# Kernel tuning notes

Hardware: AMD Instinct MI355X
Metric: run time of the kernel (lower is better)

## Reference

```python
import jax, jax.numpy as jnp
import numpy as np


def _bilinear(img, gy, gx):
    # img: (H,W); gy,gx: normalized grid coords in [-1,1] (torch grid_sample,
    # bilinear, zeros padding, align_corners=False semantics)
    H, W = img.shape
    y = ((gy + 1.0) * H - 1.0) * 0.5
    x = ((gx + 1.0) * W - 1.0) * 0.5
    y0 = jnp.floor(y); x0 = jnp.floor(x)
    y1 = y0 + 1.0; x1 = x0 + 1.0
    wy1 = y - y0; wx1 = x - x0
    wy0 = 1.0 - wy1; wx0 = 1.0 - wx1

    def gather(yy, xx):
        valid = (yy >= 0) & (yy < H) & (xx >= 0) & (xx < W)
        yc = jnp.clip(yy, 0, H - 1).astype(jnp.int32)
        xc = jnp.clip(xx, 0, W - 1).astype(jnp.int32)
        return jnp.where(valid, img[yc, xc], 0.0)

    return (wy0 * wx0 * gather(y0, x0) + wy0 * wx1 * gather(y0, x1)
            + wy1 * wx0 * gather(y1, x0) + wy1 * wx1 * gather(y1, x1))


_sample = jax.vmap(_bilinear)  # over frames


def setup_inputs() -> dict:
    key = jax.random.key(0)
    ks = jax.random.split(key, 10)
    nframe, batchsize = 16, 1
    H, W = 512, 640
    hp, wp = H - 128, W - 128
    # C/C_back hold pixel coordinates: channel 2i -> y in [0,H], 2i+1 -> x in [0,W]
    scale = jnp.tile(jnp.array([H, W], jnp.float32), nframe)  # (2*nframe,)
    return {
        "y_pred": jax.random.normal(ks[0], (1, nframe - 1, hp, wp), jnp.float32),
        "inp1": jax.random.normal(ks[1], (1, 2, H, W), jnp.float32),
        "inp2": jax.random.normal(ks[2], (1, 2 * nframe, H, W), jnp.float32),
        "inp2_back": jax.random.normal(ks[3], (1, 2 * nframe, H, W), jnp.float32),
        "inp7": 0.1 * jax.random.normal(ks[4], (1, 9 * (nframe - 1)), jnp.float32),
        "inp6": jax.random.normal(ks[5], (1, hp, wp), jnp.float32),
        "inp77": 0.1 * jax.random.normal(ks[6], (1, 9), jnp.float32),
        "nframe": nframe,
        "batchsize": batchsize,
        "C": jax.random.uniform(ks[7], (1, H, W, 2 * nframe), jnp.float32) * scale,
        "C_back": jax.random.uniform(ks[8], (1, H, W, 2 * nframe), jnp.float32) * scale,
        "reg": 1,
        "P1": 1,
        "P2": 1,
    }


def reference(y_pred, inp1, inp2, inp2_back, inp7, inp6, inp77, nframe,
              batchsize, C, C_back, reg, P1, P2):
    # Original torch code is only well-defined for batchsize == 1.
    _, _, H, W = inp1.shape
    hp, wp = y_pred.shape[2], y_pred.shape[3]
    PAD = 64
    dt = y_pred.dtype

    # zero-padded warped-field stacks
    y_pred1 = jnp.zeros((nframe - 1, H, W), dt).at[:, PAD:PAD + hp, PAD:PAD + wp].set(y_pred[0])
    y_pred2 = jnp.zeros((H, W), dt).at[PAD:PAD + hp, PAD:PAD + wp].set(inp6[0])

    # per-frame homography params: inp5 (9, nframe+1), last column zeros
    inp5 = jnp.concatenate([inp77[0][:, None], inp7[0].reshape(9, nframe - 1),
                            jnp.zeros((9, 1), dt)], axis=1)
    a = inp5[0] + 1.0  # (nframe+1,)
    b = inp5[3]
    c = inp5[6]

    # grids: C[..., 2i] -> y, C[..., 2i+1] -> x, normalized to [-1,1]
    Cr = jnp.moveaxis(C[0].reshape(H, W, nframe, 2), 2, 0)       # (nframe,H,W,2)
    Cb = jnp.moveaxis(C_back[0].reshape(H, W, nframe, 2), 2, 0)
    gy = (Cr[..., 0] - H / 2) / (H / 2)
    gx = (Cr[..., 1] - W / 2) / (W / 2)
    gby = (Cb[..., 0] - H / 2) / (H / 2)
    gbx = (Cb[..., 1] - W / 2) / (W / 2)

    warp5 = _sample(y_pred1, gy[:nframe - 1], gx[:nframe - 1])   # (nframe-1,H,W)
    warp6 = _sample(y_pred1, gby[1:nframe], gbx[1:nframe])       # (nframe-1,H,W)

    zero = jnp.zeros((1, H, W), dt)
    warp5f = jnp.concatenate([warp5, zero])        # frame nframe-1 has no forward warp
    warp6f = jnp.concatenate([zero, warp6])        # frame 0 has no backward warp
    prev = jnp.concatenate([y_pred2[None], y_pred1])   # i==0 uses y_pred2, else y_pred1[i-1]
    nxt = jnp.concatenate([y_pred1, zero])             # last frame term is zero

    inp2_r = inp2[0].reshape(nframe, 2, H, W)
    back_r = inp2_back[0].reshape(nframe, 2, H, W)

    ai, bi, ci = a[:nframe, None, None], b[:nframe, None, None], c[:nframe, None, None]
    an, bn, cn = a[1:, None, None], b[1:, None, None], c[1:, None, None]

    diff0 = (ai * inp1[0, 1] + bi * inp1[0, 0] + ci + prev
             - (an * inp2_r[:, 1] + bn * inp2_r[:, 0] + cn + warp5f))
    diff1 = (ai * back_r[:, 1] + bi * back_r[:, 0] + ci + warp6f
             - (an * inp1[0, 1] + bn * inp1[0, 0] + cn + nxt))

    row0 = jnp.mean(diff0.reshape(nframe, -1) ** 2, axis=1)
    row1 = jnp.mean(diff1.reshape(nframe, -1) ** 2, axis=1)
    return jnp.mean(0.5 * (row0 + row1))
```

## Files before the change

kernel.cpp:

```cpp
#include <hip/hip_runtime.h>

#define HH 512
#define WW 640
#define HP 384
#define WP 512
#define PAD 64
#define NF 16
#define HW (HH*WW)
#define PXB 128
#define NPH 8
#define NBLK (HW/PXB)
#define CSTR 34

__device__ __forceinline__ float ntload(const float* p) {
    return __builtin_nontemporal_load(p);
}

__device__ __forceinline__ float row_pair(const float* __restrict__ yp, int fbase,
                                          int iy, int ix, float wx0, float wx1) {
    if ((unsigned)iy >= HP) return 0.f;
    const float* row = yp + (size_t)(fbase + iy) * WP;
    float v0 = ((unsigned)ix      < WP) ? row[ix]     : 0.f;
    float v1 = ((unsigned)(ix+1) < WP) ? row[ix + 1] : 0.f;
    return wx0 * v0 + wx1 * v1;
}

__device__ __forceinline__ float bsample(const float* __restrict__ yp, int f, float Cy, float Cx) {
    float gy = (Cy - 256.0f) / 256.0f;
    float gx = (Cx - 320.0f) / 320.0f;
    float y = ((gy + 1.0f) * 512.0f - 1.0f) * 0.5f;
    float x = ((gx + 1.0f) * 640.0f - 1.0f) * 0.5f;
    float y0f = floorf(y), x0f = floorf(x);
    float wy1 = y - y0f, wx1 = x - x0f;
    float wy0 = 1.0f - wy1, wx0 = 1.0f - wx1;
    int y0 = (int)y0f, x0 = (int)x0f;
    int fbase = f * HP;
    int iy0 = y0 - PAD, ix0 = x0 - PAD;
    float r0 = row_pair(yp, fbase, iy0,     ix0, wx0, wx1);
    float r1 = row_pair(yp, fbase, iy0 + 1, ix0, wx0, wx1);
    return wy0 * r0 + wy1 * r1;
}

__device__ __forceinline__ void coef(const float* __restrict__ inp7,
                                     const float* __restrict__ inp77,
                                     int k, float& a, float& b, float& c) {
    if (k == 0)      { a = inp77[0] + 1.0f;  b = inp77[3];     c = inp77[6];     }
    else if (k <= 15){ a = inp7[k-1] + 1.0f; b = inp7[45+k-1]; c = inp7[90+k-1]; }
    else             { a = 1.0f;             b = 0.0f;         c = 0.0f;         }
}

__global__ __launch_bounds__(256) void verloss_main(
    const float* __restrict__ y_pred,
    const float* __restrict__ inp1,
    const float* __restrict__ inp2,
    const float* __restrict__ inp2b,
    const float* __restrict__ inp7,
    const float* __restrict__ inp6,
    const float* __restrict__ inp77,
    const float* __restrict__ C,
    const float* __restrict__ Cb,
    double* __restrict__ partial)
{
    __shared__ float sC [PXB * CSTR];
    __shared__ float sCb[PXB * CSTR];
    __shared__ double sdata[4];

    const int tid  = threadIdx.x;
    const int pxl  = tid >> 1;
    const int kloc = tid & 1;
    const int p    = blockIdx.x * PXB + pxl;

    {
        const float2* gC  = reinterpret_cast<const float2*>(C  + (size_t)blockIdx.x * PXB * 32);
        const float2* gCb = reinterpret_cast<const float2*>(Cb + (size_t)blockIdx.x * PXB * 32);
        #pragma unroll
        for (int i = 0; i < 8; ++i) {
            int f2 = tid + i * 256;
            int spx = f2 >> 4, sj = f2 & 15;
            float2 v  = gC [f2];
            float2 vb = gCb[f2];
            *reinterpret_cast<float2*>(&sC [spx * CSTR + 2 * sj]) = v;
            *reinterpret_cast<float2*>(&sCb[spx * CSTR + 2 * sj]) = vb;
        }
    }

    int y = p / WW, x = p - y * WW;
    int iy = y - PAD, ix = x - PAD;
    bool inpad = ((unsigned)iy < HP) && ((unsigned)ix < WP);
    int padoff = iy * WP + ix;
    float A = inp1[HW + p];
    float B = inp1[p];

    float acc = 0.f;
    __syncthreads();

    for (int g = 0; g < NPH; ++g) {
        int k = 2 * g + kloc;

        float ak, bk, ck, an, bn, cn;
        coef(inp7, inp77, k,     ak, bk, ck);
        coef(inp7, inp77, k + 1, an, bn, cn);

        float prev;
        if (k == 0) prev = inpad ? inp6[padoff] : 0.f;
        else        prev = inpad ? y_pred[(size_t)((k-1)*HP)*WP + padoff] : 0.f;
        float nxt = (k < NF-1 && inpad) ? y_pred[(size_t)(k*HP)*WP + padoff] : 0.f;

        float w5 = 0.f, w6 = 0.f;
        if (k < NF-1) {
            float2 gg = *reinterpret_cast<const float2*>(&sC [pxl * CSTR + 2 * k]);
            w5 = bsample(y_pred, k, gg.x, gg.y);
        }
        if (k >= 1) {
            float2 gg = *reinterpret_cast<const float2*>(&sCb[pxl * CSTR + 2 * k]);
            w6 = bsample(y_pred, k - 1, gg.x, gg.y);
        }

        float i2hi = ntload(inp2  + (size_t)(2*k+1)*HW + p);
        float i2lo = ntload(inp2  + (size_t)(2*k  )*HW + p);
        float ibhi = ntload(inp2b + (size_t)(2*k+1)*HW + p);
        float iblo = ntload(inp2b + (size_t)(2*k  )*HW + p);

        float d0 = ak*A + bk*B + ck + prev - (an*i2hi + bn*i2lo + cn + w5);
        float d1 = ak*ibhi + bk*iblo + ck + w6 - (an*A + bn*B + cn + nxt);
        acc += d0*d0 + d1*d1;

        if (g < NPH - 1) __syncthreads();
    }

    double v = (double)acc;
    #pragma unroll
    for (int off = 32; off > 0; off >>= 1) v += __shfl_down(v, off, 64);
    int wid = tid >> 6, lane = tid & 63;
    if (lane == 0) sdata[wid] = v;
    __syncthreads();
    if (tid == 0)
        partial[blockIdx.x] = sdata[0] + sdata[1] + sdata[2] + sdata[3];
}

__global__ __launch_bounds__(1024) void verloss_finalize(
    const double* __restrict__ partial, int n, float* __restrict__ out)
{
    double v = 0.0;
    for (int i = threadIdx.x; i < n; i += 1024) v += partial[i];
    #pragma unroll
    for (int off = 32; off > 0; off >>= 1) v += __shfl_down(v, off, 64);
    __shared__ double sdata[16];
    int wid = threadIdx.x >> 6, lane = threadIdx.x & 63;
    if (lane == 0) sdata[wid] = v;
    __syncthreads();
    if (threadIdx.x == 0) {
        double s = 0.0;
        #pragma unroll
        for (int i = 0; i < 16; ++i) s += sdata[i];
        out[0] = (float)(s * (0.5 / ((double)NF * HW)));
    }
}

extern "C" void kernel_launch(void* const* d_in, const int* in_sizes, int n_in,
                              void* d_out, int out_size, void* d_ws, size_t ws_size,
                              hipStream_t stream) {
    const float* y_pred = (const float*)d_in[0];
    const float* inp1   = (const float*)d_in[1];
    const float* inp2   = (const float*)d_in[2];
    const float* inp2b  = (const float*)d_in[3];
    const float* inp7   = (const float*)d_in[4];
    const float* inp6   = (const float*)d_in[5];
    const float* inp77  = (const float*)d_in[6];
    const float* C      = (const float*)d_in[9];
    const float* Cb     = (const float*)d_in[10];
    float* out = (float*)d_out;
    double* partial = (double*)d_ws;

    verloss_main<<<NBLK, 256, 0, stream>>>(y_pred, inp1, inp2, inp2b, inp7,
                                           inp6, inp77, C, Cb, partial);
    verloss_finalize<<<1, 1024, 0, stream>>>(partial, NBLK, out);
}
```

Baseline: 136.4 us.

## Vectorize bilinear row loads, drop per-phase barriers, unroll phase loop

The bilinear sampler now fetches each row's two neighbouring texels with one unaligned 8-byte load from a clamped column index, then selects the right values for edge cases, where before it issued two guarded scalar loads. The C/C_back staging loads become nontemporal. The per-iteration __syncthreads inside the phase loop is removed, since the shared arrays are only read after the single initial barrier. The phase loop is fully unrolled and launch bounds ask for 4 blocks per CU. Together these aim to cut gather instruction count and sync stalls, at the cost of higher register pressure from the unrolling and the occupancy hint.

```diff
diff --git a/kernel.cpp b/kernel.cpp
--- a/kernel.cpp
+++ b/kernel.cpp
@@ -12,17 +12,19 @@
 #define NBLK (HW/PXB)
 #define CSTR 34
 
+typedef float vf2 __attribute__((ext_vector_type(2)));
+
 __device__ __forceinline__ float ntload(const float* p) {
     return __builtin_nontemporal_load(p);
 }
+__device__ __forceinline__ vf2 ntload2(const float* p) {
+    return __builtin_nontemporal_load(reinterpret_cast<const vf2*>(p));
+}
 
-__device__ __forceinline__ float row_pair(const float* __restrict__ yp, int fbase,
-                                          int iy, int ix, float wx0, float wx1) {
-    if ((unsigned)iy >= HP) return 0.f;
-    const float* row = yp + (size_t)(fbase + iy) * WP;
-    float v0 = ((unsigned)ix      < WP) ? row[ix]     : 0.f;
-    float v1 = ((unsigned)(ix+1) < WP) ? row[ix + 1] : 0.f;
-    return wx0 * v0 + wx1 * v1;
+__device__ __forceinline__ vf2 ld2u(const float* __restrict__ p) {
+    vf2 r;
+    __builtin_memcpy(&r, p, sizeof(r));
+    return r;
 }
 
 __device__ __forceinline__ float bsample(const float* __restrict__ yp, int f, float Cy, float Cx) {
@@ -33,11 +35,25 @@
     float y0f = floorf(y), x0f = floorf(x);
     float wy1 = y - y0f, wx1 = x - x0f;
     float wy0 = 1.0f - wy1, wx0 = 1.0f - wx1;
-    int y0 = (int)y0f, x0 = (int)x0f;
-    int fbase = f * HP;
-    int iy0 = y0 - PAD, ix0 = x0 - PAD;
-    float r0 = row_pair(yp, fbase, iy0,     ix0, wx0, wx1);
-    float r1 = row_pair(yp, fbase, iy0 + 1, ix0, wx0, wx1);
+    int iy0 = (int)y0f - PAD;
+    int ix  = (int)x0f - PAD;
+    int ixc = min(max(ix, 0), WP - 2);
+    int d   = ix - ixc;
+
+    const float* base = yp + (size_t)f * HP * WP + ixc;
+    float r0 = 0.f, r1 = 0.f;
+    if ((unsigned)iy0 < HP) {
+        vf2 v = ld2u(base + (size_t)iy0 * WP);
+        float v0 = (d == 0) ? v.x : ((d == 1)  ? v.y : 0.f);
+        float v1 = (d == 0) ? v.y : ((d == -1) ? v.x : 0.f);
+        r0 = wx0 * v0 + wx1 * v1;
+    }
+    if ((unsigned)(iy0 + 1) < HP) {
+        vf2 v = ld2u(base + (size_t)(iy0 + 1) * WP);
+        float v0 = (d == 0) ? v.x : ((d == 1)  ? v.y : 0.f);
+        float v1 = (d == 0) ? v.y : ((d == -1) ? v.x : 0.f);
+        r1 = wx0 * v0 + wx1 * v1;
+    }
     return wy0 * r0 + wy1 * r1;
 }
 
@@ -49,7 +65,7 @@
     else             { a = 1.0f;             b = 0.0f;         c = 0.0f;         }
 }
 
-__global__ __launch_bounds__(256) void verloss_main(
+__global__ __launch_bounds__(256, 4) void verloss_main(
     const float* __restrict__ y_pred,
     const float* __restrict__ inp1,
     const float* __restrict__ inp2,
@@ -71,16 +87,16 @@
     const int p    = blockIdx.x * PXB + pxl;
 
     {
-        const float2* gC  = reinterpret_cast<const float2*>(C  + (size_t)blockIdx.x * PXB * 32);
-        const float2* gCb = reinterpret_cast<const float2*>(Cb + (size_t)blockIdx.x * PXB * 32);
+        const float* gC  = C  + (size_t)blockIdx.x * PXB * 32;
+        const float* gCb = Cb + (size_t)blockIdx.x * PXB * 32;
         #pragma unroll
         for (int i = 0; i < 8; ++i) {
             int f2 = tid + i * 256;
             int spx = f2 >> 4, sj = f2 & 15;
-            float2 v  = gC [f2];
-            float2 vb = gCb[f2];
-            *reinterpret_cast<float2*>(&sC [spx * CSTR + 2 * sj]) = v;
-            *reinterpret_cast<float2*>(&sCb[spx * CSTR + 2 * sj]) = vb;
+            vf2 v  = ntload2(gC  + 2 * f2);
+            vf2 vb = ntload2(gCb + 2 * f2);
+            *reinterpret_cast<vf2*>(&sC [spx * CSTR + 2 * sj]) = v;
+            *reinterpret_cast<vf2*>(&sCb[spx * CSTR + 2 * sj]) = vb;
         }
     }
 
@@ -94,6 +110,7 @@
     float acc = 0.f;
     __syncthreads();
 
+    #pragma unroll
     for (int g = 0; g < NPH; ++g) {
         int k = 2 * g + kloc;
 
@@ -108,11 +125,11 @@
 
         float w5 = 0.f, w6 = 0.f;
         if (k < NF-1) {
-            float2 gg = *reinterpret_cast<const float2*>(&sC [pxl * CSTR + 2 * k]);
+            vf2 gg = *reinterpret_cast<const vf2*>(&sC [pxl * CSTR + 2 * k]);
             w5 = bsample(y_pred, k, gg.x, gg.y);
         }
         if (k >= 1) {
-            float2 gg = *reinterpret_cast<const float2*>(&sCb[pxl * CSTR + 2 * k]);
+            vf2 gg = *reinterpret_cast<const vf2*>(&sCb[pxl * CSTR + 2 * k]);
             w6 = bsample(y_pred, k - 1, gg.x, gg.y);
         }
 
@@ -124,8 +141,6 @@
         float d0 = ak*A + bk*B + ck + prev - (an*i2hi + bn*i2lo + cn + w5);
         float d1 = ak*ibhi + bk*iblo + ck + w6 - (an*A + bn*B + cn + nxt);
         acc += d0*d0 + d1*d1;
-
-        if (g < NPH - 1) __syncthreads();
     }
 
     double v = (double)acc;
```

Result: slower. 174.7 us (+28.1%).
